# Kernel tuning notes

Measured on AMD Instinct MI355X. Metric: run time of the kernel, lower is better.

The kernel has to match this reference:

```python
import jax, jax.numpy as jnp
import numpy as np

B, L, D = 16384, 5, 1024  # batch, lesionNum, feat_dim == att_dim
LN_EPS = 1e-5


def _layernorm(x, g, b):
    mu = jnp.mean(x, axis=-1, keepdims=True)
    var = jnp.var(x, axis=-1, keepdims=True)
    return (x - mu) * jax.lax.rsqrt(var + LN_EPS) * g + b


def setup_inputs() -> dict:
    key = jax.random.key(0)
    ks = jax.random.split(key, 8)
    s = 0.02
    x = jax.random.normal(ks[0], (B, L, D), dtype=jnp.float32)
    mask = jax.random.randint(ks[1], (1, L), 0, 2, dtype=jnp.int64)
    mask = mask.at[0, 0].set(1)  # guarantee at least one unmasked position
    Wq = jax.random.normal(ks[2], (D, D), dtype=jnp.float32) * s
    Wk = jax.random.normal(ks[3], (D, D), dtype=jnp.float32) * s
    Wv = jax.random.normal(ks[4], (D, D), dtype=jnp.float32) * s
    W1 = jax.random.normal(ks[5], (D, D), dtype=jnp.float32) * s
    b1 = jnp.zeros((D,), dtype=jnp.float32)
    W2 = jax.random.normal(ks[6], (D, D), dtype=jnp.float32) * s
    b2 = jnp.zeros((D,), dtype=jnp.float32)
    att_g = jnp.ones((D,), dtype=jnp.float32)
    att_b = jnp.zeros((D,), dtype=jnp.float32)
    ff_g = jnp.ones((D,), dtype=jnp.float32)
    ff_b = jnp.zeros((D,), dtype=jnp.float32)
    return dict(x=x, mask=mask, Wq=Wq, Wk=Wk, Wv=Wv, W1=W1, b1=b1, W2=W2,
                b2=b2, att_g=att_g, att_b=att_b, ff_g=ff_g, ff_b=ff_b)


def reference(x, mask, Wq, Wk, Wv, W1, b1, W2, b2, att_g, att_b, ff_g, ff_b):
    # QKV (no bias). With nhead=1 the reshape makes scores per-token dot
    # products: (B,L,1,D) @ (B,L,D,1) -> (B,L,1,1); we keep them as (B,L).
    q = jnp.einsum('bld,ed->ble', x, Wq)
    k = jnp.einsum('bld,ed->ble', x, Wk)
    v = jnp.einsum('bld,ed->ble', x, Wv)
    scores = jnp.sum(q * k, axis=-1) / jnp.sqrt(jnp.float32(D))  # (B,L)
    # torch loop sets -inf where ANY mask row has 0 (applied to all batches)
    keep = jnp.all(mask != 0, axis=0)  # (L,)
    scores = jnp.where(keep[None, :], scores, -jnp.inf)
    probs = jax.nn.softmax(scores, axis=1)  # softmax over token dim (dim=1)
    probs = jnp.where(jnp.isnan(probs), 0.0, probs)  # nan-safe (all-masked)
    attn = probs[:, :, None] * v  # (B,L,1,1)@(B,L,1,D) == per-token scaling
    y = _layernorm(attn + x, att_g, att_b)
    # FFN: Linear -> exact GELU -> Linear (dropout inactive in eval)
    h = jax.nn.gelu(jnp.einsum('bld,ed->ble', y, W1) + b1, approximate=False)
    ff = jnp.einsum('bld,ed->ble', h, W2) + b2
    return _layernorm(ff + y, ff_g, ff_b)
```

## Files before the change

### kernel.cpp

```cpp
#include <hip/hip_runtime.h>
#include <hip/hip_bf16.h>
#include <cstdint>


typedef float f32x4 __attribute__((ext_vector_type(4)));
typedef __bf16 bf16x8 __attribute__((ext_vector_type(8)));

#define DD 1024
#define NROWS 81920L

__device__ __forceinline__ unsigned short f2bf(float f) {
  union { float f; unsigned u; } c; c.f = f;
  unsigned u = c.u;
  return (unsigned short)((u + 0x7FFFu + ((u >> 16) & 1u)) >> 16);
}
__device__ __forceinline__ float bf2f(unsigned short b) {
  union { unsigned u; float f; } c; c.u = ((unsigned)b) << 16;
  return c.f;
}
__device__ __forceinline__ void unpack8(uint4 v, float* o) {
  o[0] = bf2f((unsigned short)(v.x & 0xffffu)); o[1] = bf2f((unsigned short)(v.x >> 16));
  o[2] = bf2f((unsigned short)(v.y & 0xffffu)); o[3] = bf2f((unsigned short)(v.y >> 16));
  o[4] = bf2f((unsigned short)(v.z & 0xffffu)); o[5] = bf2f((unsigned short)(v.z >> 16));
  o[6] = bf2f((unsigned short)(v.w & 0xffffu)); o[7] = bf2f((unsigned short)(v.w >> 16));
}
__device__ __forceinline__ void gload_lds16(const void* g, void* l) {
  __builtin_amdgcn_global_load_lds(
      (const __attribute__((address_space(1))) unsigned int*)g,
      (__attribute__((address_space(3))) unsigned int*)l, 16, 0, 0);
}

__global__ void __launch_bounds__(256) k_cvt_bf16(const float* __restrict__ in,
                                                  unsigned short* __restrict__ out, long n) {
  long i = ((long)blockIdx.x * blockDim.x + threadIdx.x) * 8;
  long stride = (long)gridDim.x * blockDim.x * 8;
  for (; i < n; i += stride) {
    f32x4 a = *(const f32x4*)(in + i);
    f32x4 b = *(const f32x4*)(in + i + 4);
    uint4 o;
    o.x = (unsigned)f2bf(a[0]) | ((unsigned)f2bf(a[1]) << 16);
    o.y = (unsigned)f2bf(a[2]) | ((unsigned)f2bf(a[3]) << 16);
    o.z = (unsigned)f2bf(b[0]) | ((unsigned)f2bf(b[1]) << 16);
    o.w = (unsigned)f2bf(b[2]) | ((unsigned)f2bf(b[3]) << 16);
    *(uint4*)(out + i) = o;
  }
}

__global__ void __launch_bounds__(256) k_gt(const float* __restrict__ Wq,
                                            const float* __restrict__ Wk,
                                            unsigned short* __restrict__ Gt) {
  __shared__ float sk[16][16];
  __shared__ float sq[16][64];
  const int tx = threadIdx.x, ty = threadIdx.y;
  const int n0 = blockIdx.y * 16;
  const int k0 = blockIdx.x * 64;
  float acc[4] = {0.f, 0.f, 0.f, 0.f};
  for (int e0 = 0; e0 < 1024; e0 += 16) {
    sk[ty][tx] = Wk[(long)(e0 + ty) * DD + n0 + tx];
    *(f32x4*)&sq[ty][tx * 4] = *(const f32x4*)&Wq[(long)(e0 + ty) * DD + k0 + tx * 4];
    __syncthreads();
#pragma unroll
    for (int ee = 0; ee < 16; ++ee) {
      float kv = sk[ee][ty];
      f32x4 qv = *(const f32x4*)&sq[ee][tx * 4];
      acc[0] += kv * qv[0]; acc[1] += kv * qv[1];
      acc[2] += kv * qv[2]; acc[3] += kv * qv[3];
    }
    __syncthreads();
  }
  uint2 o;
  o.x = (unsigned)f2bf(acc[0]) | ((unsigned)f2bf(acc[1]) << 16);
  o.y = (unsigned)f2bf(acc[2]) | ((unsigned)f2bf(acc[3]) << 16);
  *(uint2*)&Gt[(long)(n0 + ty) * DD + k0 + tx * 4] = o;
}

#define VMBAR(N)                                             \
  do {                                                       \
    asm volatile("s_waitcnt vmcnt(" #N ")" ::: "memory");    \
    __builtin_amdgcn_s_barrier();                            \
    asm volatile("" ::: "memory");                           \
  } while (0)

template <int EPI>
__global__ void __launch_bounds__(512, 2) k_gemm256(
    const unsigned short* __restrict__ A,
    const unsigned short* __restrict__ B,
    unsigned short* __restrict__ outb,
    float* __restrict__ outf,
    const float* __restrict__ bias,
    const unsigned short* __restrict__ resid,
    const int ntl2,
    const int cst) {
  __shared__ __align__(16) char ldsB[131072];
  const int tid = threadIdx.x;
  const int lane = tid & 63;
  const int wid = tid >> 6;
  const int wm = wid >> 2, wn = wid & 3;

  const int nwg = gridDim.x;
  const int cpx = nwg >> 3;
  const int d = blockIdx.x;
  const int l = (d & 7) * cpx + (d >> 3);
  const int mt = l >> ntl2;
  const int nt = l & ((1 << ntl2) - 1);
  const long m0 = (long)mt * 256;
  const int n0 = nt * 256;

  const int r0off = tid * 16;
  const int r1off = 8192 + tid * 16;
  const int rw0 = r0off >> 6, rw1 = r1off >> 6;
  const int oc0 = (r0off & 63) ^ (((rw0 >> 1) & 3) << 4);
  const int oc1 = (r1off & 63) ^ (((rw1 >> 1) & 3) << 4);
  const char* sA0 = (const char*)A + (m0 + rw0) * 2048 + oc0;
  const char* sA1 = (const char*)A + (m0 + rw1) * 2048 + oc1;
  const char* sB0 = (const char*)B + (long)(n0 + rw0) * 2048 + oc0;
  const char* sB1 = (const char*)B + (long)(n0 + rw1) * 2048 + oc1;

  const int la = lane & 15, lg = lane >> 4;
  const int cb = ((lg ^ ((la >> 1) & 3)) << 4);
  int aoff[8], boff[4];
#pragma unroll
  for (int mi = 0; mi < 8; ++mi) aoff[mi] = (wm * 128 + mi * 16 + la) * 64 + cb;
#pragma unroll
  for (int nj = 0; nj < 4; ++nj) boff[nj] = (wn * 64 + nj * 16 + la) * 64 + cb;

  f32x4 acc[8][4];
#pragma unroll
  for (int mi = 0; mi < 8; ++mi)
#pragma unroll
    for (int nj = 0; nj < 4; ++nj) acc[mi][nj] = f32x4{0.f, 0.f, 0.f, 0.f};

  auto stageA = [&](int kt) {
    char* base = ldsB + ((kt & 3) << 15);
    const long ko = (long)kt << 6;
    gload_lds16(sA0 + ko, base + r0off);
    gload_lds16(sA1 + ko, base + r1off);
  };
  auto stageB = [&](int kt) {
    char* base = ldsB + ((kt & 3) << 15) + 16384;
    const long ko = (long)kt << 6;
    gload_lds16(sB0 + ko, base + r0off);
    gload_lds16(sB1 + ko, base + r1off);
  };

  auto tile = [&](int kt, bool st) {
    const char* bA = ldsB + ((kt & 3) << 15);
    const char* bB = bA + 16384;
    bf16x8 fa[4], fb[4];
#pragma unroll
    for (int i = 0; i < 4; ++i) fa[i] = *(const bf16x8*)(bA + aoff[i]);
#pragma unroll
    for (int j = 0; j < 4; ++j) fb[j] = *(const bf16x8*)(bB + boff[j]);
    if (st) stageA(kt + 3);
    __builtin_amdgcn_s_barrier();
    asm volatile("s_waitcnt lgkmcnt(0)" ::: "memory");
    __builtin_amdgcn_sched_barrier(0);
    __builtin_amdgcn_s_setprio(1);
#pragma unroll
    for (int i = 0; i < 4; ++i)
#pragma unroll
      for (int j = 0; j < 4; ++j)
        acc[i][j] = __builtin_amdgcn_mfma_f32_16x16x32_bf16(fa[i], fb[j], acc[i][j], 0, 0, 0);
    __builtin_amdgcn_s_setprio(0);
    __builtin_amdgcn_s_barrier();
#pragma unroll
    for (int i = 0; i < 4; ++i) fa[i] = *(const bf16x8*)(bA + aoff[4 + i]);
    if (st) stageB(kt + 3);
    __builtin_amdgcn_s_barrier();
    asm volatile("s_waitcnt lgkmcnt(0)" ::: "memory");
    __builtin_amdgcn_sched_barrier(0);
    __builtin_amdgcn_s_setprio(1);
#pragma unroll
    for (int i = 0; i < 4; ++i)
#pragma unroll
      for (int j = 0; j < 4; ++j)
        acc[4 + i][j] = __builtin_amdgcn_mfma_f32_16x16x32_bf16(fa[i], fb[j], acc[4 + i][j], 0, 0, 0);
    __builtin_amdgcn_s_setprio(0);
  };

  stageA(0); stageB(0); stageA(1); stageB(1); stageA(2); stageB(2);
  VMBAR(8);

  for (int kt = 0; kt < 29; ++kt) {
    tile(kt, true);
    VMBAR(8);
  }
  tile(29, false); VMBAR(4);
  tile(30, false); VMBAR(0);
  tile(31, false);

  const long rbase = m0 + wm * 128 + (lane >> 4) * 4;
  const int cbase = n0 + wn * 64 + la;
#pragma unroll
  for (int mi = 0; mi < 8; ++mi) {
#pragma unroll
    for (int nj = 0; nj < 4; ++nj) {
      const int col = cbase + nj * 16;
      float bv = 0.f;
      if constexpr (EPI != 0) bv = bias[col];
#pragma unroll
      for (int t = 0; t < 4; ++t) {
        const long r = rbase + mi * 16 + t;
        float v = acc[mi][nj][t];
        if constexpr (EPI == 0) {
          outb[r * (long)cst + col] = f2bf(v);
        } else if constexpr (EPI == 1) {
          v += bv;
          v = 0.5f * v * (1.0f + erff(v * 0.70710678118654752f));
          outb[r * (long)cst + col] = f2bf(v);
        } else if constexpr (EPI == 2) {
          v += bv + bf2f(resid[r * (long)cst + col]);
          outf[r * (long)cst + col] = v;
        } else {
          v += bv + bf2f(resid[r * (long)cst + col]);
          outb[r * (long)cst + col] = f2bf(v);
        }
      }
    }
  }
}

__global__ void __launch_bounds__(256) k_attn_ln(
    const unsigned short* __restrict__ xb, const unsigned short* __restrict__ uv,
    unsigned short* __restrict__ yb, const int* __restrict__ mask,
    const float* __restrict__ att_g, const float* __restrict__ att_b) {
  const int b = blockIdx.x * 4 + (threadIdx.x >> 6);
  const int lane = threadIdx.x & 63;
  const long xbase = (long)b * 5120 + lane * 16;
  const long ubase = (long)b * 10240 + lane * 16;

  float xr[5][16];
  float sc[5];
#pragma unroll
  for (int l = 0; l < 5; ++l) {
    const unsigned short* xp = xb + xbase + l * 1024;
    const unsigned short* up = uv + ubase + l * 2048;
    unpack8(*(const uint4*)xp, xr[l]); unpack8(*(const uint4*)(xp + 8), xr[l] + 8);
    float uu[16];
    unpack8(*(const uint4*)up, uu); unpack8(*(const uint4*)(up + 8), uu + 8);
    float d = 0.f;
#pragma unroll
    for (int c = 0; c < 16; ++c) d += xr[l][c] * uu[c];
#pragma unroll
    for (int off = 32; off; off >>= 1) d += __shfl_xor(d, off);
    sc[l] = d * 0.03125f;
  }
  bool keep[5];
  float m = -1e30f;
#pragma unroll
  for (int l = 0; l < 5; ++l) {
    keep[l] = (mask[l] != 0);
    if (keep[l]) m = fmaxf(m, sc[l]);
  }
  float p[5], s = 0.f;
#pragma unroll
  for (int l = 0; l < 5; ++l) {
    p[l] = keep[l] ? __expf(sc[l] - m) : 0.f;
    s += p[l];
  }
  const float inv = 1.f / s;

  float gg[16], bb[16];
  {
    const float* gp = att_g + lane * 16;
    const float* bp = att_b + lane * 16;
#pragma unroll
    for (int q = 0; q < 4; ++q) {
      f32x4 gv = *(const f32x4*)(gp + q * 4);
      f32x4 bv = *(const f32x4*)(bp + q * 4);
#pragma unroll
      for (int c = 0; c < 4; ++c) { gg[q * 4 + c] = gv[c]; bb[q * 4 + c] = bv[c]; }
    }
  }

#pragma unroll
  for (int l = 0; l < 5; ++l) {
    const unsigned short* vp = uv + ubase + l * 2048 + 1024;
    float vv[16];
    unpack8(*(const uint4*)vp, vv); unpack8(*(const uint4*)(vp + 8), vv + 8);
    const float pl = p[l] * inv;
    float t[16], sm = 0.f, sq = 0.f;
#pragma unroll
    for (int c = 0; c < 16; ++c) {
      t[c] = pl * vv[c] + xr[l][c];
      sm += t[c];
      sq += t[c] * t[c];
    }
#pragma unroll
    for (int off = 32; off; off >>= 1) {
      sm += __shfl_xor(sm, off);
      sq += __shfl_xor(sq, off);
    }
    const float mu = sm * (1.f / 1024.f);
    const float var = sq * (1.f / 1024.f) - mu * mu;
    const float rs = rsqrtf(var + 1e-5f);
    unsigned short r[16];
#pragma unroll
    for (int c = 0; c < 16; ++c) r[c] = f2bf((t[c] - mu) * rs * gg[c] + bb[c]);
    uint4 o0, o1;
    o0.x = (unsigned)r[0] | ((unsigned)r[1] << 16);  o0.y = (unsigned)r[2] | ((unsigned)r[3] << 16);
    o0.z = (unsigned)r[4] | ((unsigned)r[5] << 16);  o0.w = (unsigned)r[6] | ((unsigned)r[7] << 16);
    o1.x = (unsigned)r[8] | ((unsigned)r[9] << 16);  o1.y = (unsigned)r[10] | ((unsigned)r[11] << 16);
    o1.z = (unsigned)r[12] | ((unsigned)r[13] << 16); o1.w = (unsigned)r[14] | ((unsigned)r[15] << 16);
    unsigned short* yp = yb + xbase + l * 1024;
    *(uint4*)yp = o0;
    *(uint4*)(yp + 8) = o1;
  }
}

__global__ void __launch_bounds__(256) k_ln_final(float* __restrict__ z,
                                                  const float* __restrict__ g,
                                                  const float* __restrict__ bb) {
  const int lane = threadIdx.x & 63;
  const long row = (long)blockIdx.x * 4 + (threadIdx.x >> 6);
  float* p = z + row * DD + lane * 16;
  f32x4 v[4];
  float sm = 0.f, sq = 0.f;
#pragma unroll
  for (int q = 0; q < 4; ++q) {
    v[q] = *(const f32x4*)(p + q * 4);
#pragma unroll
    for (int c = 0; c < 4; ++c) { sm += v[q][c]; sq += v[q][c] * v[q][c]; }
  }
#pragma unroll
  for (int off = 32; off; off >>= 1) {
    sm += __shfl_xor(sm, off);
    sq += __shfl_xor(sq, off);
  }
  const float mu = sm * (1.f / 1024.f);
  const float var = sq * (1.f / 1024.f) - mu * mu;
  const float rs = rsqrtf(var + 1e-5f);
  const float* gp = g + lane * 16;
  const float* bp = bb + lane * 16;
#pragma unroll
  for (int q = 0; q < 4; ++q) {
    f32x4 gv = *(const f32x4*)(gp + q * 4);
    f32x4 bv = *(const f32x4*)(bp + q * 4);
#pragma unroll
    for (int c = 0; c < 4; ++c) v[q][c] = (v[q][c] - mu) * rs * gv[c] + bv[c];
    *(f32x4*)(p + q * 4) = v[q];
  }
}

__global__ void __launch_bounds__(256) k_ln_final_bf(const unsigned short* __restrict__ zb,
                                                     float* __restrict__ out,
                                                     const float* __restrict__ g,
                                                     const float* __restrict__ bb) {
  const int lane = threadIdx.x & 63;
  const long row = (long)blockIdx.x * 4 + (threadIdx.x >> 6);
  const unsigned short* p = zb + row * DD + lane * 16;
  float t[16];
  unpack8(*(const uint4*)p, t);
  unpack8(*(const uint4*)(p + 8), t + 8);
  float sm = 0.f, sq = 0.f;
#pragma unroll
  for (int c = 0; c < 16; ++c) { sm += t[c]; sq += t[c] * t[c]; }
#pragma unroll
  for (int off = 32; off; off >>= 1) {
    sm += __shfl_xor(sm, off);
    sq += __shfl_xor(sq, off);
  }
  const float mu = sm * (1.f / 1024.f);
  const float var = sq * (1.f / 1024.f) - mu * mu;
  const float rs = rsqrtf(var + 1e-5f);
  float* op = out + row * DD + lane * 16;
  const float* gp = g + lane * 16;
  const float* bp = bb + lane * 16;
#pragma unroll
  for (int q = 0; q < 4; ++q) {
    f32x4 gv = *(const f32x4*)(gp + q * 4);
    f32x4 bv = *(const f32x4*)(bp + q * 4);
    f32x4 o;
#pragma unroll
    for (int c = 0; c < 4; ++c) o[c] = (t[q * 4 + c] - mu) * rs * gv[c] + bv[c];
    *(f32x4*)(op + q * 4) = o;
  }
}

extern "C" void kernel_launch(void* const* d_in, const int* in_sizes, int n_in,
                              void* d_out, int out_size, void* d_ws, size_t ws_size,
                              hipStream_t stream) {
  const float* x     = (const float*)d_in[0];
  const int*   mask  = (const int*)d_in[1];
  const float* Wq    = (const float*)d_in[2];
  const float* Wk    = (const float*)d_in[3];
  const float* Wv    = (const float*)d_in[4];
  const float* W1    = (const float*)d_in[5];
  const float* b1    = (const float*)d_in[6];
  const float* W2    = (const float*)d_in[7];
  const float* b2    = (const float*)d_in[8];
  const float* att_g = (const float*)d_in[9];
  const float* att_b = (const float*)d_in[10];
  const float* ff_g  = (const float*)d_in[11];
  const float* ff_b  = (const float*)d_in[12];

  const long NE = NROWS * DD;
  unsigned short* xb   = (unsigned short*)d_ws;
  unsigned short* hb   = xb + NE;
  unsigned short* Bcat = hb + NE;
  unsigned short* W1b  = Bcat + 2L * DD * DD;
  unsigned short* W2b  = W1b + (long)DD * DD;
  unsigned short* zb   = W2b + (long)DD * DD;

  const size_t need_zb = (size_t)(3L * NE + 4L * DD * DD) * 2;
  const bool use_zb = ws_size >= need_zb;

  unsigned short* uvb = (unsigned short*)d_out;
  float* outf = (float*)d_out;

  k_cvt_bf16<<<2048, 256, 0, stream>>>(x, xb, NE);
  k_cvt_bf16<<<512, 256, 0, stream>>>(Wv, Bcat + (long)DD * DD, (long)DD * DD);
  k_cvt_bf16<<<512, 256, 0, stream>>>(W1, W1b, (long)DD * DD);
  k_cvt_bf16<<<512, 256, 0, stream>>>(W2, W2b, (long)DD * DD);
  k_gt<<<dim3(16, 64), dim3(16, 16), 0, stream>>>(Wq, Wk, Bcat);

  k_gemm256<0><<<2560, 512, 0, stream>>>(xb, Bcat, uvb, nullptr, nullptr, nullptr, 3, 2048);
  k_attn_ln<<<4096, 256, 0, stream>>>(xb, uvb, xb, mask, att_g, att_b);
  k_gemm256<1><<<1280, 512, 0, stream>>>(xb, W1b, hb, nullptr, b1, nullptr, 2, 1024);
  if (use_zb) {
    k_gemm256<3><<<1280, 512, 0, stream>>>(hb, W2b, zb, nullptr, b2, xb, 2, 1024);
    k_ln_final_bf<<<20480, 256, 0, stream>>>(zb, outf, ff_g, ff_b);
  } else {
    k_gemm256<2><<<1280, 512, 0, stream>>>(hb, W2b, nullptr, outf, b2, xb, 2, 1024);
    k_ln_final<<<20480, 256, 0, stream>>>(outf, ff_g, ff_b);
  }
}
```

Measured before the change: 1.269 ms.

## Restructure GEMM main loop with register double-buffered LDS fragments

Rewrites the 256x256 GEMM k-loop so that the LDS fragments for the next k-tile are read into a second register set while MFMAs run on the current one. Each k-tile now needs one barrier instead of three. All four global-to-LDS loads are issued together per stage. The XOR swizzle on LDS rows is removed for a plain row-major layout, which simplifies addressing but can bring back LDS bank conflicts on the 64-byte-stride fragment reads. Holding two fragment sets also raises register pressure at 2 waves per SIMD.

```diff
diff --git a/kernel.cpp b/kernel.cpp
--- a/kernel.cpp
+++ b/kernel.cpp
@@ -74,12 +74,29 @@
   *(uint2*)&Gt[(long)(n0 + ty) * DD + k0 + tx * 4] = o;
 }
 
-#define VMBAR(N)                                             \
-  do {                                                       \
-    asm volatile("s_waitcnt vmcnt(" #N ")" ::: "memory");    \
-    __builtin_amdgcn_s_barrier();                            \
-    asm volatile("" ::: "memory");                           \
-  } while (0)
+
+#define TILE(T, RSLOT, SSLOT, CA, CB, NA, NB, DOREAD, DOSTAGE, VM4)            \
+  {                                                                            \
+    if (VM4) { asm volatile("s_waitcnt vmcnt(4)" ::: "memory"); }              \
+    else     { asm volatile("s_waitcnt vmcnt(0)" ::: "memory"); }              \
+    __builtin_amdgcn_s_barrier();                                              \
+    asm volatile("" ::: "memory");                                             \
+    if (DOREAD) {                                                              \
+      const char* bn_ = ldsB + (RSLOT) * 32768;                                \
+      _Pragma("unroll") for (int mi = 0; mi < 8; ++mi)                         \
+        NA[mi] = *(const bf16x8*)(bn_ + aoff[mi]);                             \
+      _Pragma("unroll") for (int nj = 0; nj < 4; ++nj)                         \
+        NB[nj] = *(const bf16x8*)(bn_ + 16384 + boff[nj]);                     \
+    }                                                                          \
+    if (DOSTAGE) stage((T) + 3, ldsB + (SSLOT) * 32768);                       \
+    __builtin_amdgcn_sched_barrier(0);                                         \
+    __builtin_amdgcn_s_setprio(1);                                             \
+    _Pragma("unroll") for (int mi = 0; mi < 8; ++mi)                           \
+      _Pragma("unroll") for (int nj = 0; nj < 4; ++nj)                         \
+        acc[mi][nj] = __builtin_amdgcn_mfma_f32_16x16x32_bf16(                 \
+            CA[mi], CB[nj], acc[mi][nj], 0, 0, 0);                             \
+    __builtin_amdgcn_s_setprio(0);                                             \
+  }
 
 template <int EPI>
 __global__ void __launch_bounds__(512, 2) k_gemm256(
@@ -99,30 +116,35 @@
 
   const int nwg = gridDim.x;
   const int cpx = nwg >> 3;
-  const int d = blockIdx.x;
-  const int l = (d & 7) * cpx + (d >> 3);
-  const int mt = l >> ntl2;
-  const int nt = l & ((1 << ntl2) - 1);
+  const int dd = blockIdx.x;
+  const int lgc = (dd & 7) * cpx + (dd >> 3);
+  const int mt = lgc >> ntl2;
+  const int nt = lgc & ((1 << ntl2) - 1);
   const long m0 = (long)mt * 256;
   const int n0 = nt * 256;
 
-  const int r0off = tid * 16;
-  const int r1off = 8192 + tid * 16;
-  const int rw0 = r0off >> 6, rw1 = r1off >> 6;
-  const int oc0 = (r0off & 63) ^ (((rw0 >> 1) & 3) << 4);
-  const int oc1 = (r1off & 63) ^ (((rw1 >> 1) & 3) << 4);
-  const char* sA0 = (const char*)A + (m0 + rw0) * 2048 + oc0;
-  const char* sA1 = (const char*)A + (m0 + rw1) * 2048 + oc1;
-  const char* sB0 = (const char*)B + (long)(n0 + rw0) * 2048 + oc0;
-  const char* sB1 = (const char*)B + (long)(n0 + rw1) * 2048 + oc1;
+  const int srow = tid >> 2;
+  const int scol = (tid & 3) * 16;
+  const char* gA0 = (const char*)A + (m0 + srow) * 2048 + scol;
+  const char* gA1 = gA0 + 128 * 2048;
+  const char* gB0 = (const char*)B + ((long)n0 + srow) * 2048 + scol;
+  const char* gB1 = gB0 + 128 * 2048;
+  const int d0 = tid * 16;
+
+  auto stage = [&](int kt, char* base) {
+    const long ko = (long)kt << 6;
+    gload_lds16(gA0 + ko, base + d0);
+    gload_lds16(gA1 + ko, base + 8192 + d0);
+    gload_lds16(gB0 + ko, base + 16384 + d0);
+    gload_lds16(gB1 + ko, base + 24576 + d0);
+  };
 
   const int la = lane & 15, lg = lane >> 4;
-  const int cb = ((lg ^ ((la >> 1) & 3)) << 4);
   int aoff[8], boff[4];
 #pragma unroll
-  for (int mi = 0; mi < 8; ++mi) aoff[mi] = (wm * 128 + mi * 16 + la) * 64 + cb;
-#pragma unroll
-  for (int nj = 0; nj < 4; ++nj) boff[nj] = (wn * 64 + nj * 16 + la) * 64 + cb;
+  for (int mi = 0; mi < 8; ++mi) aoff[mi] = (wm * 128 + mi * 16 + la) * 64 + lg * 16;
+#pragma unroll
+  for (int nj = 0; nj < 4; ++nj) boff[nj] = (wn * 64 + nj * 16 + la) * 64 + lg * 16;
 
   f32x4 acc[8][4];
 #pragma unroll
@@ -130,64 +152,29 @@
 #pragma unroll
     for (int nj = 0; nj < 4; ++nj) acc[mi][nj] = f32x4{0.f, 0.f, 0.f, 0.f};
 
-  auto stageA = [&](int kt) {
-    char* base = ldsB + ((kt & 3) << 15);
-    const long ko = (long)kt << 6;
-    gload_lds16(sA0 + ko, base + r0off);
-    gload_lds16(sA1 + ko, base + r1off);
-  };
-  auto stageB = [&](int kt) {
-    char* base = ldsB + ((kt & 3) << 15) + 16384;
-    const long ko = (long)kt << 6;
-    gload_lds16(sB0 + ko, base + r0off);
-    gload_lds16(sB1 + ko, base + r1off);
-  };
-
-  auto tile = [&](int kt, bool st) {
-    const char* bA = ldsB + ((kt & 3) << 15);
-    const char* bB = bA + 16384;
-    bf16x8 fa[4], fb[4];
-#pragma unroll
-    for (int i = 0; i < 4; ++i) fa[i] = *(const bf16x8*)(bA + aoff[i]);
-#pragma unroll
-    for (int j = 0; j < 4; ++j) fb[j] = *(const bf16x8*)(bB + boff[j]);
-    if (st) stageA(kt + 3);
-    __builtin_amdgcn_s_barrier();
-    asm volatile("s_waitcnt lgkmcnt(0)" ::: "memory");
-    __builtin_amdgcn_sched_barrier(0);
-    __builtin_amdgcn_s_setprio(1);
-#pragma unroll
-    for (int i = 0; i < 4; ++i)
-#pragma unroll
-      for (int j = 0; j < 4; ++j)
-        acc[i][j] = __builtin_amdgcn_mfma_f32_16x16x32_bf16(fa[i], fb[j], acc[i][j], 0, 0, 0);
-    __builtin_amdgcn_s_setprio(0);
-    __builtin_amdgcn_s_barrier();
-#pragma unroll
-    for (int i = 0; i < 4; ++i) fa[i] = *(const bf16x8*)(bA + aoff[4 + i]);
-    if (st) stageB(kt + 3);
-    __builtin_amdgcn_s_barrier();
-    asm volatile("s_waitcnt lgkmcnt(0)" ::: "memory");
-    __builtin_amdgcn_sched_barrier(0);
-    __builtin_amdgcn_s_setprio(1);
-#pragma unroll
-    for (int i = 0; i < 4; ++i)
-#pragma unroll
-      for (int j = 0; j < 4; ++j)
-        acc[4 + i][j] = __builtin_amdgcn_mfma_f32_16x16x32_bf16(fa[i], fb[j], acc[4 + i][j], 0, 0, 0);
-    __builtin_amdgcn_s_setprio(0);
-  };
-
-  stageA(0); stageB(0); stageA(1); stageB(1); stageA(2); stageB(2);
-  VMBAR(8);
-
-  for (int kt = 0; kt < 29; ++kt) {
-    tile(kt, true);
-    VMBAR(8);
-  }
-  tile(29, false); VMBAR(4);
-  tile(30, false); VMBAR(0);
-  tile(31, false);
+  stage(0, ldsB);
+  stage(1, ldsB + 32768);
+  stage(2, ldsB + 65536);
+  asm volatile("s_waitcnt vmcnt(8)" ::: "memory");
+  __builtin_amdgcn_s_barrier();
+  asm volatile("" ::: "memory");
+
+  bf16x8 a0[8], b0[4], a1[8], b1[4];
+#pragma unroll
+  for (int mi = 0; mi < 8; ++mi) a0[mi] = *(const bf16x8*)(ldsB + aoff[mi]);
+#pragma unroll
+  for (int nj = 0; nj < 4; ++nj) b0[nj] = *(const bf16x8*)(ldsB + 16384 + boff[nj]);
+
+  for (int t0 = 0; t0 < 28; t0 += 4) {
+    TILE(t0 + 0, 1, 3, a0, b0, a1, b1, true, true, true);
+    TILE(t0 + 1, 2, 0, a1, b1, a0, b0, true, true, true);
+    TILE(t0 + 2, 3, 1, a0, b0, a1, b1, true, true, true);
+    TILE(t0 + 3, 0, 2, a1, b1, a0, b0, true, true, true);
+  }
+  TILE(28, 1, 3, a0, b0, a1, b1, true, true, true);
+  TILE(29, 2, 0, a1, b1, a0, b0, true, false, true);
+  TILE(30, 3, 1, a0, b0, a1, b1, true, false, false);
+  TILE(31, 0, 2, a1, b1, a0, b0, false, false, false);
 
   const long rbase = m0 + wm * 128 + (lane >> 4) * 4;
   const int cbase = n0 + wn * 64 + la;
@@ -308,40 +295,6 @@
   }
 }
 
-__global__ void __launch_bounds__(256) k_ln_final(float* __restrict__ z,
-                                                  const float* __restrict__ g,
-                                                  const float* __restrict__ bb) {
-  const int lane = threadIdx.x & 63;
-  const long row = (long)blockIdx.x * 4 + (threadIdx.x >> 6);
-  float* p = z + row * DD + lane * 16;
-  f32x4 v[4];
-  float sm = 0.f, sq = 0.f;
-#pragma unroll
-  for (int q = 0; q < 4; ++q) {
-    v[q] = *(const f32x4*)(p + q * 4);
-#pragma unroll
-    for (int c = 0; c < 4; ++c) { sm += v[q][c]; sq += v[q][c] * v[q][c]; }
-  }
-#pragma unroll
-  for (int off = 32; off; off >>= 1) {
-    sm += __shfl_xor(sm, off);
-    sq += __shfl_xor(sq, off);
-  }
-  const float mu = sm * (1.f / 1024.f);
-  const float var = sq * (1.f / 1024.f) - mu * mu;
-  const float rs = rsqrtf(var + 1e-5f);
-  const float* gp = g + lane * 16;
-  const float* bp = bb + lane * 16;
-#pragma unroll
-  for (int q = 0; q < 4; ++q) {
-    f32x4 gv = *(const f32x4*)(gp + q * 4);
-    f32x4 bv = *(const f32x4*)(bp + q * 4);
-#pragma unroll
-    for (int c = 0; c < 4; ++c) v[q][c] = (v[q][c] - mu) * rs * gv[c] + bv[c];
-    *(f32x4*)(p + q * 4) = v[q];
-  }
-}
-
 __global__ void __launch_bounds__(256) k_ln_final_bf(const unsigned short* __restrict__ zb,
                                                      float* __restrict__ out,
                                                      const float* __restrict__ g,
@@ -374,6 +327,40 @@
 #pragma unroll
     for (int c = 0; c < 4; ++c) o[c] = (t[q * 4 + c] - mu) * rs * gv[c] + bv[c];
     *(f32x4*)(op + q * 4) = o;
+  }
+}
+
+__global__ void __launch_bounds__(256) k_ln_final(float* __restrict__ z,
+                                                  const float* __restrict__ g,
+                                                  const float* __restrict__ bb) {
+  const int lane = threadIdx.x & 63;
+  const long row = (long)blockIdx.x * 4 + (threadIdx.x >> 6);
+  float* p = z + row * DD + lane * 16;
+  f32x4 v[4];
+  float sm = 0.f, sq = 0.f;
+#pragma unroll
+  for (int q = 0; q < 4; ++q) {
+    v[q] = *(const f32x4*)(p + q * 4);
+#pragma unroll
+    for (int c = 0; c < 4; ++c) { sm += v[q][c]; sq += v[q][c] * v[q][c]; }
+  }
+#pragma unroll
+  for (int off = 32; off; off >>= 1) {
+    sm += __shfl_xor(sm, off);
+    sq += __shfl_xor(sq, off);
+  }
+  const float mu = sm * (1.f / 1024.f);
+  const float var = sq * (1.f / 1024.f) - mu * mu;
+  const float rs = rsqrtf(var + 1e-5f);
+  const float* gp = g + lane * 16;
+  const float* bp = bb + lane * 16;
+#pragma unroll
+  for (int q = 0; q < 4; ++q) {
+    f32x4 gv = *(const f32x4*)(gp + q * 4);
+    f32x4 bv = *(const f32x4*)(bp + q * 4);
+#pragma unroll
+    for (int c = 0; c < 4; ++c) v[q][c] = (v[q][c] - mu) * rs * gv[c] + bv[c];
+    *(f32x4*)(p + q * 4) = v[q];
   }
 }
 
```

Result: slower. 1.305 ms (+2.8%).
